# Optimization experiments

Measured on AMD Instinct MI355X. Metric: run time of the kernel, lower is better.

## Reference

```python
import jax, jax.numpy as jnp
import numpy as np

IH, IW, HEADS, DIM_HEAD = 32, 32, 8, 48
N = IH * IW
SCALE = DIM_HEAD ** -0.5
EPS = 1e-5


def _relative_index():
    # static precompute of relative distance indices, shape [N, N] int32
    yy, xx = np.meshgrid(np.arange(IH), np.arange(IW), indexing='ij')
    coords = np.stack([yy.ravel(), xx.ravel()])  # [2, N]
    rel = coords[:, :, None] - coords[:, None, :]  # [2, N, N]
    dist = np.ceil(np.sqrt(rel[0] ** 2 + rel[1] ** 2)).astype(np.int32)
    return jnp.asarray(dist)

REL_INDEX = _relative_index()


def _layernorm(x, w, b):
    mu = jnp.mean(x, axis=-1, keepdims=True)
    var = jnp.var(x, axis=-1, keepdims=True)
    return (x - mu) * jax.lax.rsqrt(var + EPS) * w + b


def setup_inputs() -> dict:
    key = jax.random.key(0)
    ks = jax.random.split(key, 8)
    d, inner, hid = 384, HEADS * DIM_HEAD, 1536
    return {
        'x': jax.random.normal(ks[0], (16, IH, IW, d), jnp.float32),
        'ln1_w': jnp.ones((d,), jnp.float32),
        'ln1_b': jnp.zeros((d,), jnp.float32),
        'w_qkv': jax.random.normal(ks[1], (d, 3 * inner), jnp.float32) * (d ** -0.5),
        'bias_table': jax.random.normal(ks[2], (45, HEADS), jnp.float32) * 0.02,
        'w_out': jax.random.normal(ks[3], (inner, d), jnp.float32) * (inner ** -0.5),
        'b_out': jnp.zeros((d,), jnp.float32),
        'ln2_w': jnp.ones((d,), jnp.float32),
        'ln2_b': jnp.zeros((d,), jnp.float32),
        'w1': jax.random.normal(ks[4], (d, hid), jnp.float32) * (d ** -0.5),
        'b1': jnp.zeros((hid,), jnp.float32),
        'w2': jax.random.normal(ks[5], (hid, d), jnp.float32) * (hid ** -0.5),
        'b2': jnp.zeros((d,), jnp.float32),
    }


def reference(x, ln1_w, ln1_b, w_qkv, bias_table, w_out, b_out,
              ln2_w, ln2_b, w1, b1, w2, b2):
    b = x.shape[0]
    xt = x.reshape(b, N, -1)  # b (ih iw) c

    # --- attention branch (PreNorm) ---
    h = _layernorm(xt, ln1_w, ln1_b)
    qkv = h @ w_qkv  # [b, N, 3*inner]
    q, k, v = jnp.split(qkv, 3, axis=-1)
    q = q.reshape(b, N, HEADS, DIM_HEAD).transpose(0, 2, 1, 3)
    k = k.reshape(b, N, HEADS, DIM_HEAD).transpose(0, 2, 1, 3)
    v = v.reshape(b, N, HEADS, DIM_HEAD).transpose(0, 2, 1, 3)
    dots = jnp.einsum('bhnd,bhmd->bhnm', q, k) * SCALE
    rel_bias = bias_table[REL_INDEX]  # [N, N, heads] gather
    dots = dots + rel_bias.transpose(2, 0, 1)[None]  # [1, h, N, N]
    attn = jax.nn.softmax(dots, axis=-1)
    out = jnp.einsum('bhnm,bhmd->bhnd', attn, v)
    out = out.transpose(0, 2, 1, 3).reshape(b, N, HEADS * DIM_HEAD)
    out = out @ w_out + b_out
    xt = xt + out

    # --- FFN branch (PreNorm) ---
    h = _layernorm(xt, ln2_w, ln2_b)
    h = jax.nn.gelu(h @ w1 + b1, approximate=False) @ w2 + b2
    xt = xt + h
    return xt.reshape(x.shape)
```

## Files before the change

### kernel.cpp

```cpp
#include <hip/hip_runtime.h>
#include <hip/hip_bf16.h>
#include <math.h>

typedef __bf16 bf16;
typedef __bf16 bf16x8 __attribute__((ext_vector_type(8)));
typedef __bf16 bf16x4 __attribute__((ext_vector_type(4)));
typedef __bf16 bf16x2 __attribute__((ext_vector_type(2)));
typedef float  f32x4  __attribute__((ext_vector_type(4)));

#define D_MODEL 384
#define HID     1536
#define NSEQ    1024
#define ROWS    16384
#define HEADS   8
#define DH      48
#define SCALE   0.14433756729740643f
#define MFIX    8.0f
#define BT2_N   2016
#define KVT     4608
#define QP_BH   (NSEQ * DH)
#define KP_BH   (16 * KVT)

__device__ __forceinline__ void gload16(const void* g, void* l) {
    __builtin_amdgcn_global_load_lds((const __attribute__((address_space(1))) void*)g,
                                     (__attribute__((address_space(3))) void*)l, 16, 0, 0);
}

__device__ __forceinline__ float fast_gelu(float x) {
    float u = 0.7978845608f * fmaf(0.044715f * x * x, x, x);
    float e = __expf(2.f * u);
    float t = 1.f - 2.f * __builtin_amdgcn_rcpf(e + 1.f);
    return 0.5f * x * (1.f + t);
}

__device__ __forceinline__ void wtrans_body(const float* __restrict__ in,
                                            bf16* __restrict__ out, int K, int N,
                                            int bx, int by, float (*T)[65])
{
    const int k0 = by * 64, n0 = bx * 64;
    const int rr = threadIdx.x >> 4, rc = threadIdx.x & 15;
#pragma unroll
    for (int i = 0; i < 4; ++i) {
        float4 v = *(const float4*)(in + (size_t)(k0 + rr + i * 16) * N + n0 + rc * 4);
        T[rr + i * 16][rc * 4 + 0] = v.x;  T[rr + i * 16][rc * 4 + 1] = v.y;
        T[rr + i * 16][rc * 4 + 2] = v.z;  T[rr + i * 16][rc * 4 + 3] = v.w;
    }
    __syncthreads();
#pragma unroll
    for (int i = 0; i < 4; ++i) {
        int n = rr + i * 16, kc = rc * 4;
        bf16x4 o;
        o[0] = (bf16)T[kc + 0][n];  o[1] = (bf16)T[kc + 1][n];
        o[2] = (bf16)T[kc + 2][n];  o[3] = (bf16)T[kc + 3][n];
        *(bf16x4*)(out + (size_t)(n0 + n) * K + k0 + kc) = o;
    }
}

__device__ __forceinline__ void ln_body(const float* __restrict__ x,
                                        const float* __restrict__ w,
                                        const float* __restrict__ b,
                                        bf16* __restrict__ out, int blk)
{
    int row  = blk * 4 + ((int)threadIdx.x >> 6);
    int lane = threadIdx.x & 63;
    const float* xr = x + (size_t)row * D_MODEL;

    float2 v[3];
    float s = 0.f, ss = 0.f;
#pragma unroll
    for (int i = 0; i < 3; ++i) {
        v[i] = *(const float2*)(xr + lane * 2 + i * 128);
        s  += v[i].x + v[i].y;
        ss += v[i].x * v[i].x + v[i].y * v[i].y;
    }
#pragma unroll
    for (int off = 32; off; off >>= 1) {
        s  += __shfl_xor(s,  off);
        ss += __shfl_xor(ss, off);
    }
    float mu   = s * (1.f / D_MODEL);
    float var  = ss * (1.f / D_MODEL) - mu * mu;
    float rstd = rsqrtf(var + 1e-5f);

    bf16* orow = out + (size_t)row * D_MODEL;
#pragma unroll
    for (int i = 0; i < 3; ++i) {
        int c = lane * 2 + i * 128;
        float2 wv = *(const float2*)(w + c);
        float2 bv = *(const float2*)(b + c);
        bf16x2 o;
        o[0] = (bf16)((v[i].x - mu) * rstd * wv.x + bv.x);
        o[1] = (bf16)((v[i].y - mu) * rstd * wv.y + bv.y);
        *(bf16x2*)(orow + c) = o;
    }
}

__global__ __launch_bounds__(256)
void prep_kernel(const float* __restrict__ w_qkv, const float* __restrict__ w_out,
                 const float* __restrict__ w1, const float* __restrict__ w2,
                 bf16* __restrict__ wqkvT, bf16* __restrict__ woutT,
                 bf16* __restrict__ w1T, bf16* __restrict__ w2T,
                 bf16* __restrict__ Kp, bf16* __restrict__ Vp,
                 const float* __restrict__ bias_table, float* __restrict__ Btab,
                 const float* __restrict__ x, const float* __restrict__ ln1_w,
                 const float* __restrict__ ln1_b, bf16* __restrict__ regB)
{
    __shared__ float T[64][65];
    const int bid = blockIdx.x, tid = threadIdx.x;

    if (bid < 432) {
        const float* in; bf16* outp; int K, N, nx, local;
        if (bid < 108)      { in = w_qkv; outp = wqkvT; K = 384;  N = 1152; local = bid;       nx = 18; }
        else if (bid < 144) { in = w_out; outp = woutT; K = 384;  N = 384;  local = bid - 108; nx = 6;  }
        else if (bid < 288) { in = w1;    outp = w1T;   K = 384;  N = 1536; local = bid - 144; nx = 24; }
        else                { in = w2;    outp = w2T;   K = 1536; N = 384;  local = bid - 288; nx = 6;  }
        wtrans_body(in, outp, K, N, local % nx, local / nx, T);
    } else if (bid < 1072) {
        const int pb = bid - 432;
        if (pb < 512) {
            int row = pb * 256 + tid;
            bf16x8 z = {};
            bf16* p = Kp + (size_t)row * 72 + 48;
            *(bf16x8*)(p) = z;  *(bf16x8*)(p + 8) = z;  *(bf16x8*)(p + 16) = z;
        } else {
            int idx = (pb - 512) * 256 + tid;
            int tile = idx >> 4, rr = idx & 15;
            bf16 o = (bf16)1.f;
            bf16x8 ones = {o, o, o, o, o, o, o, o};
            bf16* p = Vp + (size_t)tile * KVT + (48 + rr) * 72;
#pragma unroll
            for (int c = 0; c < 9; ++c) *(bf16x8*)(p + c * 8) = ones;
        }
    } else if (bid < 1080) {
        int idx = (bid - 1072) * 256 + tid;
        if (idx < BT2_N) {
            int dy = idx / 63, dx = idx % 63 - 31;
            int s2 = dy * dy + dx * dx;
            int r = (int)ceilf(sqrtf((float)s2));
            while (r * r < s2) ++r;
            while (r > 0 && (r - 1) * (r - 1) >= s2) --r;
#pragma unroll
            for (int h = 0; h < HEADS; ++h)
                Btab[h * BT2_N + idx] = bias_table[r * HEADS + h] - MFIX;
        }
    } else {
        ln_body(x, ln1_w, ln1_b, regB, bid - 1080);
    }
}

__global__ __launch_bounds__(256)
void ln_kernel(const float* __restrict__ x, const float* __restrict__ w,
               const float* __restrict__ b, bf16* __restrict__ out)
{
    ln_body(x, w, b, out, blockIdx.x);
}

template<int EPI, typename CT>
__global__ __launch_bounds__(256)
void gemm3_kernel(const bf16* __restrict__ A, const bf16* __restrict__ BT,
                  CT* __restrict__ C, const float* __restrict__ bias,
                  const float* __restrict__ res, int nxblk, int Nn, int K,
                  bf16* __restrict__ qp, bf16* __restrict__ kp, bf16* __restrict__ vp)
{
    __shared__ alignas(16) bf16 As[128][64];
    __shared__ alignas(16) bf16 Bs[128][64];

    const int bid  = blockIdx.x;
    const int xcd  = bid & 7;
    const int slot = bid >> 3;
    const int yy   = slot / nxblk;
    const int m0   = (yy * 8 + xcd) * 128;
    const int n0   = (slot - yy * nxblk) * 128;

    const int tid  = threadIdx.x;
    const int w    = tid >> 6;
    const int lane = tid & 63;
    const int quad = lane >> 4;
    const int l16  = lane & 15;

    const int srow = lane >> 3;
    const int scol = (lane & 7) * 8;

    f32x4 acc[4][4] = {};

    for (int kt = 0; kt < K; kt += 64) {
        __syncthreads();
#pragma unroll
        for (int c = 0; c < 4; ++c) {
            const int ch = w * 4 + c;
            gload16(A  + (size_t)(m0 + ch * 8 + srow) * K + kt + scol, &As[ch * 8][0]);
            gload16(BT + (size_t)(n0 + ch * 8 + srow) * K + kt + scol, &Bs[ch * 8][0]);
        }
        __syncthreads();

#pragma unroll
        for (int kk = 0; kk < 2; ++kk) {
            bf16x8 af[4], bfr[4];
#pragma unroll
            for (int mt = 0; mt < 4; ++mt)
                af[mt] = *(const bf16x8*)(&As[(w & 1) * 64 + mt * 16 + l16][kk * 32 + quad * 8]);
#pragma unroll
            for (int nt = 0; nt < 4; ++nt)
                bfr[nt] = *(const bf16x8*)(&Bs[(w >> 1) * 64 + nt * 16 + l16][kk * 32 + quad * 8]);
#pragma unroll
            for (int mt = 0; mt < 4; ++mt)
#pragma unroll
                for (int nt = 0; nt < 4; ++nt)
                    acc[mt][nt] = __builtin_amdgcn_mfma_f32_16x16x32_bf16(
                        af[mt], bfr[nt], acc[mt][nt], 0, 0, 0);
        }
    }

#pragma unroll
    for (int mt = 0; mt < 4; ++mt) {
#pragma unroll
        for (int nt = 0; nt < 4; ++nt) {
            const int c0 = n0 + (w >> 1) * 64 + nt * 16;
            const int c  = c0 + l16;
            float bi = (EPI == 1 || EPI == 2) ? bias[c] : 0.f;
#pragma unroll
            for (int r = 0; r < 4; ++r) {
                int row = m0 + (w & 1) * 64 + mt * 16 + quad * 4 + r;
                float v = acc[mt][nt][r] + bi;
                if (EPI == 1) {
                    v += res[(size_t)row * Nn + c];
                    C[(size_t)row * Nn + c] = (CT)v;
                } else if (EPI == 2) {
                    v = fast_gelu(v);
                    C[(size_t)row * Nn + c] = (CT)v;
                } else {
                    int b   = row >> 10, seq = row & 1023;
                    if (c0 < 384) {
                        int h = c / 48, d = c - h * 48;
                        qp[(size_t)(b * 8 + h) * QP_BH + seq * 48 + d] = (bf16)(v * SCALE);
                    } else if (c0 < 768) {
                        int ck = c - 384;
                        int h = ck / 48, d = ck - h * 48;
                        kp[(size_t)(b * 8 + h) * KP_BH + (seq >> 6) * KVT
                           + (seq & 63) * 72 + d] = (bf16)v;
                    } else {
                        int cv = c - 768;
                        int h = cv / 48, d = cv - h * 48;
                        vp[(size_t)(b * 8 + h) * KP_BH + (seq >> 6) * KVT
                           + d * 72 + (seq & 63)] = (bf16)v;
                    }
                }
            }
        }
    }
}

__global__ __launch_bounds__(512)
void attn_kernel(const bf16* __restrict__ Qp, const bf16* __restrict__ Kp,
                 const bf16* __restrict__ Vp, const float* __restrict__ Btab,
                 bf16* __restrict__ out)
{
    __shared__ alignas(16) bf16 Ks[128][72];
    __shared__ alignas(16) bf16 Vs[2][64][72];
    __shared__ alignas(16) bf16 Ps[8][2][16][72];
    __shared__ alignas(16) float B2f[BT2_N];

    const int bid  = blockIdx.x;
    const int xcd  = bid & 7;
    const int slot = bid >> 3;
    const int qc   = slot & 3;
    const int bh   = (slot >> 2) * 8 + xcd;
    const int q0   = qc * 256;
    const int tid  = threadIdx.x;
    const int wave = tid >> 6;
    const int lane = tid & 63;
    const int quad = lane >> 4;
    const int l16  = lane & 15;
    const int b    = bh >> 3, h = bh & 7;

    {
        const char* src = (const char*)(Btab + (size_t)h * BT2_N);
        int off = tid * 16;
        if (off < BT2_N * 4)
            gload16(src + off, (char*)B2f + wave * 1024);
    }

    bf16x8 qf0[2], qf1[2];
    int qy[2], qxp[2];
#pragma unroll
    for (int s = 0; s < 2; ++s) {
        int qrow = q0 + s * 128 + wave * 16 + l16;
        const bf16* qptr = Qp + (size_t)bh * QP_BH + qrow * 48;
        qf0[s] = *(const bf16x8*)(qptr + quad * 8);
#pragma unroll
        for (int c = 0; c < 8; ++c) qf1[s][c] = (bf16)0.f;
        if (quad < 2) qf1[s] = *(const bf16x8*)(qptr + 32 + quad * 8);
        qy[s]  = qrow >> 5;
        qxp[s] = (qrow & 31) + 31;
    }

    f32x4 o_acc[2][4] = {};

    for (int t = 0; t < 8; ++t) {
        const bf16* kbase = Kp + (size_t)(bh * 16 + 2 * t) * KVT;
        const bf16* vbase = Vp + (size_t)(bh * 16 + 2 * t) * KVT;
        __syncthreads();
        for (int i = wave; i < 18; i += 8) {
            gload16(kbase + i * 512 + lane * 8, (bf16*)Ks + i * 512);
            gload16(vbase + i * 512 + lane * 8, (bf16*)&Vs[0][0][0] + i * 512);
        }
        __syncthreads();

#pragma unroll
        for (int hf = 0; hf < 2; ++hf) {
            const int n0 = t * 128 + hf * 64;

            f32x4 sa[2][4] = {};
#pragma unroll
            for (int nt = 0; nt < 4; ++nt) {
                bf16x8 a0 = *(const bf16x8*)(&Ks[hf * 64 + nt * 16 + l16][quad * 8]);
                bf16x8 a1 = *(const bf16x8*)(&Ks[hf * 64 + nt * 16 + l16][32 + quad * 8]);
#pragma unroll
                for (int s = 0; s < 2; ++s) {
                    sa[s][nt] = __builtin_amdgcn_mfma_f32_16x16x32_bf16(a0, qf0[s], sa[s][nt], 0, 0, 0);
                    sa[s][nt] = __builtin_amdgcn_mfma_f32_16x16x32_bf16(a1, qf1[s], sa[s][nt], 0, 0, 0);
                }
            }

#pragma unroll
            for (int s = 0; s < 2; ++s)
#pragma unroll
                for (int nt = 0; nt < 4; ++nt) {
                    const int j0 = n0 + nt * 16 + quad * 4;
                    int dy  = qy[s] - (j0 >> 5);
                    int iay = dy < 0 ? -dy : dy;
                    const int ib0 = iay * 63 + qxp[s] - (j0 & 31);
                    bf16x4 pk;
#pragma unroll
                    for (int r = 0; r < 4; ++r)
                        pk[r] = (bf16)__expf(sa[s][nt][r] + B2f[ib0 - r]);
                    *(bf16x4*)(&Ps[wave][s][l16][nt * 16 + quad * 4]) = pk;
                }

#pragma unroll
            for (int kk = 0; kk < 2; ++kk) {
                bf16x8 vf[4];
#pragma unroll
                for (int d = 0; d < 4; ++d)
                    vf[d] = *(const bf16x8*)(&Vs[hf][d * 16 + l16][kk * 32 + quad * 8]);
#pragma unroll
                for (int s = 0; s < 2; ++s) {
                    bf16x8 pf = *(const bf16x8*)(&Ps[wave][s][l16][kk * 32 + quad * 8]);
#pragma unroll
                    for (int d = 0; d < 4; ++d)
                        o_acc[s][d] = __builtin_amdgcn_mfma_f32_16x16x32_bf16(
                            pf, vf[d], o_acc[s][d], 0, 0, 0);
                }
            }
        }
    }

#pragma unroll
    for (int s = 0; s < 2; ++s)
#pragma unroll
        for (int r = 0; r < 4; ++r) {
            float inv = 1.f / o_acc[s][3][r];
            int row = q0 + s * 128 + wave * 16 + quad * 4 + r;
            bf16* orow = out + ((size_t)b * NSEQ + row) * D_MODEL + h * DH;
#pragma unroll
            for (int d = 0; d < 3; ++d)
                orow[d * 16 + l16] = (bf16)(o_acc[s][d][r] * inv);
        }
}

extern "C" void kernel_launch(void* const* d_in, const int* in_sizes, int n_in,
                              void* d_out, int out_size, void* d_ws, size_t ws_size,
                              hipStream_t stream)
{
    const float* x          = (const float*)d_in[0];
    const float* ln1_w      = (const float*)d_in[1];
    const float* ln1_b      = (const float*)d_in[2];
    const float* w_qkv      = (const float*)d_in[3];
    const float* bias_table = (const float*)d_in[4];
    const float* w_out      = (const float*)d_in[5];
    const float* b_out      = (const float*)d_in[6];
    const float* ln2_w      = (const float*)d_in[7];
    const float* ln2_b      = (const float*)d_in[8];
    const float* w1         = (const float*)d_in[9];
    const float* b1         = (const float*)d_in[10];
    const float* w2         = (const float*)d_in[11];
    const float* b2         = (const float*)d_in[12];
    float* out = (float*)d_out;

    bf16* regA  = (bf16*)d_ws;
    bf16* Qpack = regA;
    bf16* Kpack = regA + 6291456;
    bf16* Vpack = regA + 15728640;
    bf16* regB  = regA + (size_t)ROWS * HID;
    bf16* wqkvT = regB + (size_t)ROWS * D_MODEL;
    bf16* woutT = wqkvT + 1152 * 384;
    bf16* w1T   = woutT + 384 * 384;
    bf16* w2T   = w1T + 1536 * 384;
    float* Btab = (float*)(w2T + 384 * 1536);
    float* x1   = out;

    prep_kernel<<<5176, 256, 0, stream>>>(
        w_qkv, w_out, w1, w2, wqkvT, woutT, w1T, w2T,
        Kpack, Vpack, bias_table, Btab, x, ln1_w, ln1_b, regB);
    gemm3_kernel<3, bf16><<<(1152 / 128) * (ROWS / 128), 256, 0, stream>>>(
        regB, wqkvT, (bf16*)nullptr, nullptr, nullptr, 1152 / 128, 1152, D_MODEL,
        Qpack, Kpack, Vpack);
    attn_kernel<<<512, 512, 0, stream>>>(Qpack, Kpack, Vpack, Btab, regB);
    gemm3_kernel<1, float><<<(D_MODEL / 128) * (ROWS / 128), 256, 0, stream>>>(
        regB, woutT, x1, b_out, x, D_MODEL / 128, D_MODEL, D_MODEL,
        nullptr, nullptr, nullptr);
    ln_kernel<<<ROWS / 4, 256, 0, stream>>>(x1, ln2_w, ln2_b, regB);
    gemm3_kernel<2, bf16><<<(HID / 128) * (ROWS / 128), 256, 0, stream>>>(
        regB, w1T, regA, b1, nullptr, HID / 128, HID, D_MODEL,
        nullptr, nullptr, nullptr);
    gemm3_kernel<1, float><<<(D_MODEL / 128) * (ROWS / 128), 256, 0, stream>>>(
        regA, w2T, out, b2, x1, D_MODEL / 128, D_MODEL, HID,
        nullptr, nullptr, nullptr);
}
```

Measured before the change: 307.9 us.

## Double-buffer K/V tiles in attention kernel to overlap loads with compute

Replaces the load-all-then-compute loop over 128-key tiles with a 64-key double-buffered pipeline. The next K/V tile is prefetched via global_load_lds into the alternate buffer while the current tile is processed, synchronised with s_waitcnt vmcnt and raw s_barrier. This aims to hide global memory latency behind the MFMA and exp work. The cost is twice as many barriers per key, and only 6 waves issue loads.

```diff
diff --git a/kernel.cpp b/kernel.cpp
--- a/kernel.cpp
+++ b/kernel.cpp
@@ -255,7 +255,7 @@
                  const bf16* __restrict__ Vp, const float* __restrict__ Btab,
                  bf16* __restrict__ out)
 {
-    __shared__ alignas(16) bf16 Ks[128][72];
+    __shared__ alignas(16) bf16 Ks[2][64][72];
     __shared__ alignas(16) bf16 Vs[2][64][72];
     __shared__ alignas(16) bf16 Ps[8][2][16][72];
     __shared__ alignas(16) float B2f[BT2_N];
@@ -296,63 +296,80 @@
 
     f32x4 o_acc[2][4] = {};
 
-    for (int t = 0; t < 8; ++t) {
-        const bf16* kbase = Kp + (size_t)(bh * 16 + 2 * t) * KVT;
-        const bf16* vbase = Vp + (size_t)(bh * 16 + 2 * t) * KVT;
-        __syncthreads();
-        for (int i = wave; i < 18; i += 8) {
-            gload16(kbase + i * 512 + lane * 8, (bf16*)Ks + i * 512);
-            gload16(vbase + i * 512 + lane * 8, (bf16*)&Vs[0][0][0] + i * 512);
-        }
-        __syncthreads();
-
-#pragma unroll
-        for (int hf = 0; hf < 2; ++hf) {
-            const int n0 = t * 128 + hf * 64;
-
-            f32x4 sa[2][4] = {};
+    auto STAGE = [&](int tt, int bufsel) {
+        if (wave < 6) {
+            const bf16* kb = Kp + (size_t)(bh * 16 + tt) * KVT;
+            const bf16* vb = Vp + (size_t)(bh * 16 + tt) * KVT;
+#pragma unroll
+            for (int j = 0; j < 3; ++j) {
+                int i = wave * 3 + j;
+                if (i < 9) gload16(kb + i * 512 + lane * 8,
+                                   (bf16*)&Ks[bufsel][0][0] + i * 512);
+                else       gload16(vb + (i - 9) * 512 + lane * 8,
+                                   (bf16*)&Vs[bufsel][0][0] + (i - 9) * 512);
+            }
+        }
+    };
+
+    STAGE(0, 0);
+
+    for (int t = 0; t < 16; ++t) {
+        const int cur = t & 1;
+        if (t < 15) {
+            STAGE(t + 1, cur ^ 1);
+            asm volatile("s_waitcnt vmcnt(3)" ::: "memory");
+        } else {
+            asm volatile("s_waitcnt vmcnt(0)" ::: "memory");
+        }
+        __builtin_amdgcn_s_barrier();
+        __builtin_amdgcn_sched_barrier(0);
+
+        const int n0 = t * 64;
+
+        f32x4 sa[2][4] = {};
+#pragma unroll
+        for (int nt = 0; nt < 4; ++nt) {
+            bf16x8 a0 = *(const bf16x8*)(&Ks[cur][nt * 16 + l16][quad * 8]);
+            bf16x8 a1 = *(const bf16x8*)(&Ks[cur][nt * 16 + l16][32 + quad * 8]);
+#pragma unroll
+            for (int s = 0; s < 2; ++s) {
+                sa[s][nt] = __builtin_amdgcn_mfma_f32_16x16x32_bf16(a0, qf0[s], sa[s][nt], 0, 0, 0);
+                sa[s][nt] = __builtin_amdgcn_mfma_f32_16x16x32_bf16(a1, qf1[s], sa[s][nt], 0, 0, 0);
+            }
+        }
+
+#pragma unroll
+        for (int s = 0; s < 2; ++s)
 #pragma unroll
             for (int nt = 0; nt < 4; ++nt) {
-                bf16x8 a0 = *(const bf16x8*)(&Ks[hf * 64 + nt * 16 + l16][quad * 8]);
-                bf16x8 a1 = *(const bf16x8*)(&Ks[hf * 64 + nt * 16 + l16][32 + quad * 8]);
-#pragma unroll
-                for (int s = 0; s < 2; ++s) {
-                    sa[s][nt] = __builtin_amdgcn_mfma_f32_16x16x32_bf16(a0, qf0[s], sa[s][nt], 0, 0, 0);
-                    sa[s][nt] = __builtin_amdgcn_mfma_f32_16x16x32_bf16(a1, qf1[s], sa[s][nt], 0, 0, 0);
-                }
+                const int j0 = n0 + nt * 16 + quad * 4;
+                int dy  = qy[s] - (j0 >> 5);
+                int iay = dy < 0 ? -dy : dy;
+                const int ib0 = iay * 63 + qxp[s] - (j0 & 31);
+                bf16x4 pk;
+#pragma unroll
+                for (int r = 0; r < 4; ++r)
+                    pk[r] = (bf16)__expf(sa[s][nt][r] + B2f[ib0 - r]);
+                *(bf16x4*)(&Ps[wave][s][l16][nt * 16 + quad * 4]) = pk;
             }
 
 #pragma unroll
-            for (int s = 0; s < 2; ++s)
-#pragma unroll
-                for (int nt = 0; nt < 4; ++nt) {
-                    const int j0 = n0 + nt * 16 + quad * 4;
-                    int dy  = qy[s] - (j0 >> 5);
-                    int iay = dy < 0 ? -dy : dy;
-                    const int ib0 = iay * 63 + qxp[s] - (j0 & 31);
-                    bf16x4 pk;
-#pragma unroll
-                    for (int r = 0; r < 4; ++r)
-                        pk[r] = (bf16)__expf(sa[s][nt][r] + B2f[ib0 - r]);
-                    *(bf16x4*)(&Ps[wave][s][l16][nt * 16 + quad * 4]) = pk;
-                }
-
-#pragma unroll
-            for (int kk = 0; kk < 2; ++kk) {
-                bf16x8 vf[4];
+        for (int kk = 0; kk < 2; ++kk) {
+            bf16x8 vf[4];
+#pragma unroll
+            for (int d = 0; d < 4; ++d)
+                vf[d] = *(const bf16x8*)(&Vs[cur][d * 16 + l16][kk * 32 + quad * 8]);
+#pragma unroll
+            for (int s = 0; s < 2; ++s) {
+                bf16x8 pf = *(const bf16x8*)(&Ps[wave][s][l16][kk * 32 + quad * 8]);
 #pragma unroll
                 for (int d = 0; d < 4; ++d)
-                    vf[d] = *(const bf16x8*)(&Vs[hf][d * 16 + l16][kk * 32 + quad * 8]);
-#pragma unroll
-                for (int s = 0; s < 2; ++s) {
-                    bf16x8 pf = *(const bf16x8*)(&Ps[wave][s][l16][kk * 32 + quad * 8]);
-#pragma unroll
-                    for (int d = 0; d < 4; ++d)
-                        o_acc[s][d] = __builtin_amdgcn_mfma_f32_16x16x32_bf16(
-                            pf, vf[d], o_acc[s][d], 0, 0, 0);
-                }
+                    o_acc[s][d] = __builtin_amdgcn_mfma_f32_16x16x32_bf16(
+                        pf, vf[d], o_acc[s][d], 0, 0, 0);
             }
         }
+
+        __builtin_amdgcn_s_barrier();
     }
 
 #pragma unroll
```

After: 312.4 us. About the same (+1.5%).
